# Kernel tuning notes

Measured on AMD Instinct MI355X. Metric: run time of the kernel, lower is better.

The kernel has to match this reference:

```python
import jax, jax.numpy as jnp
import numpy as np

CAM_DIM = 3          # args().cam_dim
ROT_DIM = 6          # args().rot_dim
NJ = 22              # number of SMPL joints in the 6D pose slice
CENTER2D_THRESH = 5.0
POSE_THRESH = 2.5
N = 2048
BATCH = 32
MAP_SIZE = 64        # args().centermap_size
PARAM_DIM = CAM_DIM + NJ * ROT_DIM + 10  # 145


def rot6d_to_rotmat(x):
    """6D rotation rep -> rotation matrix via Gram-Schmidt (ROMP convention).
    x: [N, NJ*6] -> R: [N, NJ, 3, 3] (b1,b2,b3 as columns)."""
    x = x.reshape(-1, NJ, 3, 2)
    a1, a2 = x[..., 0], x[..., 1]
    b1 = a1 / jnp.linalg.norm(a1, axis=-1, keepdims=True)
    a2p = a2 - jnp.sum(b1 * a2, axis=-1, keepdims=True) * b1
    b2 = a2p / jnp.linalg.norm(a2p, axis=-1, keepdims=True)
    b3 = jnp.cross(b1, b2)
    return jnp.stack([b1, b2, b3], axis=-1)


def setup_inputs() -> dict:
    key = jax.random.key(0)
    k1, k2, k3, k4 = jax.random.split(key, 4)
    params_preds = jax.random.normal(k1, (N, PARAM_DIM), dtype=jnp.float32)
    pred_batch_ids = jax.random.randint(k2, (N,), 0, BATCH, dtype=jnp.int32)
    pred_czyxs = jax.random.randint(k3, (N, 3), 0, MAP_SIZE, dtype=jnp.int32)
    top_score = jax.random.uniform(k4, (N,), dtype=jnp.float32)
    return {"params_preds": params_preds, "pred_batch_ids": pred_batch_ids,
            "pred_czyxs": pred_czyxs, "top_score": top_score}


def reference(params_preds, pred_batch_ids, pred_czyxs, top_score):
    n = top_score.shape[0]
    pose6d = params_preds[:, CAM_DIM:CAM_DIM + NJ * ROT_DIM]

    # pairwise L2 distance of 2D centers (czyx[:,1:])
    centers = pred_czyxs[:, 1:].astype(jnp.float32)                 # [N,2]
    c_dist = jnp.linalg.norm(centers[:, None, :] - centers[None, :, :], axis=-1)
    same_batch = pred_batch_ids[:, None] == pred_batch_ids[None, :]
    c_dist = jnp.where(same_batch, c_dist, CENTER2D_THRESH + 1.0)
    similarity = c_dist <= CENTER2D_THRESH                          # [N,N] bool

    # pairwise SMPL pose L2 error: mean_j ||R_i[j] - R_k[j]||_F
    # (original goes 6D -> angle-axis -> rotmat; the roundtrip is the identity,
    #  so we compare the Gram-Schmidt rotation matrices directly)
    R = rot6d_to_rotmat(pose6d)                                     # [N,NJ,3,3]
    G = jnp.einsum('ikab,jkab->ijk', R, R)                          # [N,N,NJ]
    n2 = jnp.sum(R * R, axis=(-1, -2))                              # [N,NJ]
    d2 = jnp.clip(n2[:, None, :] + n2[None, :, :] - 2.0 * G, 0.0, None)
    pose_dist = jnp.sqrt(d2).mean(-1)                               # [N,N]

    # per-row pose suppression (vectorized form of the python loop; rows are
    # independent and the diagonal always survives since pose_dist[i,i]=0)
    similarity = similarity & (pose_dist < POSE_THRESH)

    score_map = similarity.astype(top_score.dtype) * top_score[None, :]
    nms_inds = jnp.argmax(score_map, axis=1) == jnp.arange(n)
    return score_map, nms_inds
```

## Files before the change

kernel.cpp:

```cpp
#include <hip/hip_runtime.h>

#define NJ 22
#define CAM_DIM 3

__device__ __forceinline__ void rot6(const float* __restrict__ p, float r[9]) {
    float a1x = p[0], a2x = p[1];
    float a1y = p[2], a2y = p[3];
    float a1z = p[4], a2z = p[5];
    float n1 = sqrtf(a1x*a1x + a1y*a1y + a1z*a1z);
    float b1x = a1x/n1, b1y = a1y/n1, b1z = a1z/n1;
    float d = b1x*a2x + b1y*a2y + b1z*a2z;
    float px = a2x - d*b1x, py = a2y - d*b1y, pz = a2z - d*b1z;
    float np = sqrtf(px*px + py*py + pz*pz);
    float b2x = px/np, b2y = py/np, b2z = pz/np;
    r[0]=b1x; r[1]=b1y; r[2]=b1z;
    r[3]=b2x; r[4]=b2y; r[5]=b2z;
    r[6]=b1y*b2z - b1z*b2y;
    r[7]=b1z*b2x - b1x*b2z;
    r[8]=b1x*b2y - b1y*b2x;
}

__global__ __launch_bounds__(256) void mega_kernel(
        const float* __restrict__ params,
        const int* __restrict__ batch_ids,
        const int* __restrict__ czyx,
        const float* __restrict__ ts,
        float* __restrict__ out,
        float* __restrict__ nms,
        int n, int param_dim) {
    __shared__ unsigned long long s_red[4];

    const int i    = blockIdx.x;
    const int tid  = threadIdx.x;
    const int lane = tid & 63;
    const int wid  = tid >> 6;

    const int bi  = batch_ids[i];
    const int ciy = czyx[3*i + 1];
    const int cix = czyx[3*i + 2];
    float* row = out + (size_t)i * n;

    unsigned long long best = 0ull;

    for (int base = 0; base < n; base += blockDim.x * 4) {
        int j0 = base + tid * 4;
        if (j0 >= n) continue;

        int okmask = 0;
        if (j0 + 3 < n) {
            int4 b4 = *reinterpret_cast<const int4*>(batch_ids + j0);
            const int4* cz = reinterpret_cast<const int4*>(czyx + 3*j0);
            int4 c0 = cz[0], c1 = cz[1], c2 = cz[2];
            int by[4] = {b4.x, b4.y, b4.z, b4.w};
            int yy[4] = {c0.y, c1.x, c1.w, c2.z};
            int xx[4] = {c0.z, c1.y, c2.x, c2.w};
            #pragma unroll
            for (int u = 0; u < 4; ++u) {
                int dy = yy[u] - ciy, dx = xx[u] - cix;
                if ((by[u] == bi) && (dy*dy + dx*dx <= 25)) okmask |= 1 << u;
            }
        } else {
            for (int u = 0; u < 4 && j0 + u < n; ++u) {
                int j = j0 + u;
                int dy = czyx[3*j + 1] - ciy, dx = czyx[3*j + 2] - cix;
                if ((batch_ids[j] == bi) && (dy*dy + dx*dx <= 25)) okmask |= 1 << u;
            }
        }

        int passmask = 0;
        int du = i - j0;
        if (du >= 0 && du < 4) {
            passmask |=  (1 << du);
            okmask   &= ~(1 << du);
        }

        for (;;) {
            unsigned long long pend = __ballot(okmask != 0);
            if (pend == 0ull) break;
            int leader = __ffsll((long long)pend) - 1;
            int lok = __shfl(okmask, leader);
            int u   = __ffs(lok) - 1;
            int j   = __shfl(j0, leader) + u;

            float val = 0.0f;
            if (lane < NJ) {
                const float* pi_ = params + (size_t)i * param_dim + CAM_DIM + lane * 6;
                const float* pj_ = params + (size_t)j * param_dim + CAM_DIM + lane * 6;
                float ri[9], rj[9];
                rot6(pi_, ri);
                rot6(pj_, rj);
                float g = 0.0f, ni = 0.0f, nj = 0.0f;
                #pragma unroll
                for (int a = 0; a < 9; ++a) {
                    g  += ri[a]*rj[a];
                    ni += ri[a]*ri[a];
                    nj += rj[a]*rj[a];
                }
                val = sqrtf(fmaxf(ni + nj - 2.0f*g, 0.0f));
            }
            #pragma unroll
            for (int off = 16; off > 0; off >>= 1) val += __shfl_down(val, off, 32);
            float pd = __shfl(val, 0) * (1.0f / 22.0f);

            if (lane == leader) {
                okmask &= ~(1 << u);
                if (pd < 2.5f) passmask |= 1 << u;
            }
        }

        float sc[4];
        #pragma unroll
        for (int u = 0; u < 4; ++u)
            sc[u] = ((passmask >> u) & 1) ? ts[j0 + u] : 0.0f;

        unsigned long long cand = (unsigned int)(~(unsigned int)j0);
        if (cand > best) best = cand;
        #pragma unroll
        for (int u = 0; u < 4; ++u) {
            if ((passmask >> u) & 1) {
                unsigned long long p =
                    ((unsigned long long)__float_as_uint(sc[u]) << 32) |
                    (unsigned int)(~(unsigned int)(j0 + u));
                if (p > best) best = p;
            }
        }

        if (j0 + 3 < n) {
            *reinterpret_cast<float4*>(row + j0) = make_float4(sc[0], sc[1], sc[2], sc[3]);
        } else {
            for (int u = 0; u < 4 && j0 + u < n; ++u) row[j0 + u] = sc[u];
        }
    }

    #pragma unroll
    for (int off = 32; off > 0; off >>= 1) {
        unsigned long long o = __shfl_xor(best, off);
        if (o > best) best = o;
    }
    if (lane == 0) s_red[wid] = best;
    __syncthreads();
    if (tid == 0) {
        unsigned long long b = s_red[0];
        #pragma unroll
        for (int w = 1; w < 4; ++w) if (s_red[w] > b) b = s_red[w];
        unsigned int jwin = ~(unsigned int)(b & 0xFFFFFFFFull);
        nms[i] = (jwin == (unsigned int)i) ? 1.0f : 0.0f;
    }
}

extern "C" void kernel_launch(void* const* d_in, const int* in_sizes, int n_in,
                              void* d_out, int out_size, void* d_ws, size_t ws_size,
                              hipStream_t stream) {
    const float* params = (const float*)d_in[0];
    const int*   batch  = (const int*)d_in[1];
    const int*   czyx   = (const int*)d_in[2];
    const float* ts     = (const float*)d_in[3];

    const int n = in_sizes[1];
    const int param_dim = in_sizes[0] / n;

    float* out = (float*)d_out;
    float* nms = out + (size_t)n * n;

    mega_kernel<<<n, 256, 0, stream>>>(params, batch, czyx, ts, out, nms, n, param_dim);
}
```

Baseline: 15.86 us.

## Split into gate and pose kernels with precomputed rotation matrices and hit lists

Splits the fused kernel into two. The first kernel builds each row's rotation matrices and squared norms once into workspace, writes gated scores, and records up to 64 spatial hits per row in a list. The second kernel, one wavefront per row, computes the pose distance only for those hits, zeroes suppressed entries and picks the NMS winner. This removes the repeated 6D-to-rotmat work and the wave-serialized pose loop from the bandwidth-bound output pass. In exchange it adds a second launch and workspace traffic, and rows with more than 64 hits would give wrong results.

```diff
diff --git a/kernel.cpp b/kernel.cpp
--- a/kernel.cpp
+++ b/kernel.cpp
@@ -2,6 +2,8 @@
 
 #define NJ 22
 #define CAM_DIM 3
+#define RSTRIDE 224
+#define HITCAP 64
 
 __device__ __forceinline__ void rot6(const float* __restrict__ p, float r[9]) {
     float a1x = p[0], a2x = p[1];
@@ -20,27 +22,39 @@
     r[8]=b1x*b2y - b1y*b2x;
 }
 
-__global__ __launch_bounds__(256) void mega_kernel(
+__global__ __launch_bounds__(256) void gate_kernel(
         const float* __restrict__ params,
         const int* __restrict__ batch_ids,
         const int* __restrict__ czyx,
         const float* __restrict__ ts,
         float* __restrict__ out,
-        float* __restrict__ nms,
+        float* __restrict__ ws_R,
+        int* __restrict__ ws_cnt,
+        int* __restrict__ ws_hits,
         int n, int param_dim) {
-    __shared__ unsigned long long s_red[4];
+    __shared__ int l_cnt;
+    __shared__ int l_hits[HITCAP];
 
-    const int i    = blockIdx.x;
-    const int tid  = threadIdx.x;
-    const int lane = tid & 63;
-    const int wid  = tid >> 6;
+    const int i   = blockIdx.x;
+    const int tid = threadIdx.x;
+
+    if (tid == 0) l_cnt = 0;
+
+    if (tid < NJ) {
+        float r[9];
+        rot6(params + (size_t)i * param_dim + CAM_DIM + tid * 6, r);
+        float* Ri = ws_R + (size_t)i * RSTRIDE;
+        float s = 0.0f;
+        #pragma unroll
+        for (int a = 0; a < 9; ++a) { Ri[tid*9 + a] = r[a]; s += r[a]*r[a]; }
+        Ri[198 + tid] = s;
+    }
+    __syncthreads();
 
     const int bi  = batch_ids[i];
     const int ciy = czyx[3*i + 1];
     const int cix = czyx[3*i + 2];
     float* row = out + (size_t)i * n;
-
-    unsigned long long best = 0ull;
 
     for (int base = 0; base < n; base += blockDim.x * 4) {
         int j0 = base + tid * 4;
@@ -67,83 +81,91 @@
             }
         }
 
-        int passmask = 0;
+        int pending = okmask;
         int du = i - j0;
-        if (du >= 0 && du < 4) {
-            passmask |=  (1 << du);
-            okmask   &= ~(1 << du);
-        }
-
-        for (;;) {
-            unsigned long long pend = __ballot(okmask != 0);
-            if (pend == 0ull) break;
-            int leader = __ffsll((long long)pend) - 1;
-            int lok = __shfl(okmask, leader);
-            int u   = __ffs(lok) - 1;
-            int j   = __shfl(j0, leader) + u;
-
-            float val = 0.0f;
-            if (lane < NJ) {
-                const float* pi_ = params + (size_t)i * param_dim + CAM_DIM + lane * 6;
-                const float* pj_ = params + (size_t)j * param_dim + CAM_DIM + lane * 6;
-                float ri[9], rj[9];
-                rot6(pi_, ri);
-                rot6(pj_, rj);
-                float g = 0.0f, ni = 0.0f, nj = 0.0f;
-                #pragma unroll
-                for (int a = 0; a < 9; ++a) {
-                    g  += ri[a]*rj[a];
-                    ni += ri[a]*ri[a];
-                    nj += rj[a]*rj[a];
-                }
-                val = sqrtf(fmaxf(ni + nj - 2.0f*g, 0.0f));
-            }
-            #pragma unroll
-            for (int off = 16; off > 0; off >>= 1) val += __shfl_down(val, off, 32);
-            float pd = __shfl(val, 0) * (1.0f / 22.0f);
-
-            if (lane == leader) {
-                okmask &= ~(1 << u);
-                if (pd < 2.5f) passmask |= 1 << u;
-            }
-        }
+        if (du >= 0 && du < 4) pending &= ~(1 << du);
 
         float sc[4];
         #pragma unroll
         for (int u = 0; u < 4; ++u)
-            sc[u] = ((passmask >> u) & 1) ? ts[j0 + u] : 0.0f;
-
-        unsigned long long cand = (unsigned int)(~(unsigned int)j0);
-        if (cand > best) best = cand;
-        #pragma unroll
-        for (int u = 0; u < 4; ++u) {
-            if ((passmask >> u) & 1) {
-                unsigned long long p =
-                    ((unsigned long long)__float_as_uint(sc[u]) << 32) |
-                    (unsigned int)(~(unsigned int)(j0 + u));
-                if (p > best) best = p;
-            }
-        }
+            sc[u] = ((okmask >> u) & 1) ? ts[j0 + u] : 0.0f;
 
         if (j0 + 3 < n) {
             *reinterpret_cast<float4*>(row + j0) = make_float4(sc[0], sc[1], sc[2], sc[3]);
         } else {
             for (int u = 0; u < 4 && j0 + u < n; ++u) row[j0 + u] = sc[u];
         }
+
+        while (pending) {
+            int u = __ffs(pending) - 1;
+            pending &= pending - 1;
+            int pos = atomicAdd(&l_cnt, 1);
+            if (pos < HITCAP) l_hits[pos] = j0 + u;
+        }
     }
 
-    #pragma unroll
-    for (int off = 32; off > 0; off >>= 1) {
-        unsigned long long o = __shfl_xor(best, off);
-        if (o > best) best = o;
+    __syncthreads();
+    int cnt = l_cnt < HITCAP ? l_cnt : HITCAP;
+    if (tid == 0) ws_cnt[i] = cnt;
+    for (int t = tid; t < cnt; t += blockDim.x) ws_hits[i * HITCAP + t] = l_hits[t];
+}
+
+__global__ __launch_bounds__(64) void pose_kernel(
+        const float* __restrict__ ts,
+        const float* __restrict__ ws_R,
+        const int* __restrict__ ws_cnt,
+        const int* __restrict__ ws_hits,
+        float* __restrict__ out,
+        float* __restrict__ nms,
+        int n) {
+    const int i    = blockIdx.x;
+    const int lane = threadIdx.x;
+
+    const int cnt = ws_cnt[i];
+
+    float ri[9];
+    float n2i = 0.0f;
+    if (lane < NJ) {
+        const float* Ri = ws_R + (size_t)i * RSTRIDE;
+        #pragma unroll
+        for (int a = 0; a < 9; ++a) ri[a] = Ri[lane*9 + a];
+        n2i = Ri[198 + lane];
     }
-    if (lane == 0) s_red[wid] = best;
-    __syncthreads();
-    if (tid == 0) {
-        unsigned long long b = s_red[0];
+
+    unsigned long long best =
+        ((unsigned long long)__float_as_uint(ts[i]) << 32) | (unsigned int)(~(unsigned int)i);
+    unsigned long long zfloor = (unsigned int)0xFFFFFFFFu;
+    if (zfloor > best) best = zfloor;
+
+    for (int h = 0; h < cnt; ++h) {
+        int j = ws_hits[i * HITCAP + h];
+        float val = 0.0f;
+        if (lane < NJ) {
+            const float* Rj = ws_R + (size_t)j * RSTRIDE;
+            float g = 0.0f;
+            #pragma unroll
+            for (int a = 0; a < 9; ++a) g += ri[a] * Rj[lane*9 + a];
+            float d2 = fmaxf(n2i + Rj[198 + lane] - 2.0f * g, 0.0f);
+            val = sqrtf(d2);
+        }
         #pragma unroll
-        for (int w = 1; w < 4; ++w) if (s_red[w] > b) b = s_red[w];
-        unsigned int jwin = ~(unsigned int)(b & 0xFFFFFFFFull);
+        for (int off = 16; off > 0; off >>= 1) val += __shfl_down(val, off, 32);
+        float pd = __shfl(val, 0) * (1.0f / 22.0f);
+
+        if (lane == 0) {
+            if (pd < 2.5f) {
+                unsigned long long p =
+                    ((unsigned long long)__float_as_uint(ts[j]) << 32) |
+                    (unsigned int)(~(unsigned int)j);
+                if (p > best) best = p;
+            } else {
+                out[(size_t)i * n + j] = 0.0f;
+            }
+        }
+    }
+
+    if (lane == 0) {
+        unsigned int jwin = ~(unsigned int)(best & 0xFFFFFFFFull);
         nms[i] = (jwin == (unsigned int)i) ? 1.0f : 0.0f;
     }
 }
@@ -159,8 +181,14 @@
     const int n = in_sizes[1];
     const int param_dim = in_sizes[0] / n;
 
+    float* ws_R    = (float*)d_ws;
+    int*   ws_cnt  = (int*)(ws_R + (size_t)n * RSTRIDE);
+    int*   ws_hits = ws_cnt + n;
+
     float* out = (float*)d_out;
     float* nms = out + (size_t)n * n;
 
-    mega_kernel<<<n, 256, 0, stream>>>(params, batch, czyx, ts, out, nms, n, param_dim);
+    gate_kernel<<<n, 256, 0, stream>>>(params, batch, czyx, ts, out,
+                                       ws_R, ws_cnt, ws_hits, n, param_dim);
+    pose_kernel<<<n, 64, 0, stream>>>(ts, ws_R, ws_cnt, ws_hits, out, nms, n);
 }
```

Measured after the change: 18.23 us. 14.9% more time.

## Map one wavefront per row and hoist row-i rotation out of pair loop

Applied to the files above, without the earlier changes.

Each wavefront now owns one output row and walks all columns in chunks of 256, instead of a whole 256-thread block sharing one row. This removes the shared-memory and __syncthreads reduction for the argmax. The row's rotation matrices and their squared norms are computed once per lane before the loop, so candidate pairs only evaluate rot6 for the column. The trade-off is less parallelism per row: one wave serialises the candidate processing that four waves previously split.

```diff
diff --git a/kernel.cpp b/kernel.cpp
--- a/kernel.cpp
+++ b/kernel.cpp
@@ -20,7 +20,7 @@
     r[8]=b1x*b2y - b1y*b2x;
 }
 
-__global__ __launch_bounds__(256) void mega_kernel(
+__global__ __launch_bounds__(256) void row_kernel(
         const float* __restrict__ params,
         const int* __restrict__ batch_ids,
         const int* __restrict__ czyx,
@@ -28,23 +28,28 @@
         float* __restrict__ out,
         float* __restrict__ nms,
         int n, int param_dim) {
-    __shared__ unsigned long long s_red[4];
+    const int lane = threadIdx.x & 63;
+    const int wid  = threadIdx.x >> 6;
+    const int r    = blockIdx.x * 4 + wid;
+    if (r >= n) return;
 
-    const int i    = blockIdx.x;
-    const int tid  = threadIdx.x;
-    const int lane = tid & 63;
-    const int wid  = tid >> 6;
+    const int bi  = batch_ids[r];
+    const int ciy = czyx[3*r + 1];
+    const int cix = czyx[3*r + 2];
+    float* row = out + (size_t)r * n;
 
-    const int bi  = batch_ids[i];
-    const int ciy = czyx[3*i + 1];
-    const int cix = czyx[3*i + 2];
-    float* row = out + (size_t)i * n;
+    float ri[9];
+    float n2i = 0.0f;
+    if (lane < NJ) {
+        rot6(params + (size_t)r * param_dim + CAM_DIM + lane * 6, ri);
+        #pragma unroll
+        for (int a = 0; a < 9; ++a) n2i += ri[a] * ri[a];
+    }
 
     unsigned long long best = 0ull;
 
-    for (int base = 0; base < n; base += blockDim.x * 4) {
-        int j0 = base + tid * 4;
-        if (j0 >= n) continue;
+    for (int c = 0; c < n; c += 256) {
+        int j0 = c + lane * 4;
 
         int okmask = 0;
         if (j0 + 3 < n) {
@@ -68,7 +73,7 @@
         }
 
         int passmask = 0;
-        int du = i - j0;
+        int du = r - j0;
         if (du >= 0 && du < 4) {
             passmask |=  (1 << du);
             okmask   &= ~(1 << du);
@@ -84,19 +89,15 @@
 
             float val = 0.0f;
             if (lane < NJ) {
-                const float* pi_ = params + (size_t)i * param_dim + CAM_DIM + lane * 6;
-                const float* pj_ = params + (size_t)j * param_dim + CAM_DIM + lane * 6;
-                float ri[9], rj[9];
-                rot6(pi_, ri);
-                rot6(pj_, rj);
-                float g = 0.0f, ni = 0.0f, nj = 0.0f;
+                float rj[9];
+                rot6(params + (size_t)j * param_dim + CAM_DIM + lane * 6, rj);
+                float g = 0.0f, nj = 0.0f;
                 #pragma unroll
                 for (int a = 0; a < 9; ++a) {
-                    g  += ri[a]*rj[a];
-                    ni += ri[a]*ri[a];
-                    nj += rj[a]*rj[a];
+                    g  += ri[a] * rj[a];
+                    nj += rj[a] * rj[a];
                 }
-                val = sqrtf(fmaxf(ni + nj - 2.0f*g, 0.0f));
+                val = sqrtf(fmaxf(n2i + nj - 2.0f*g, 0.0f));
             }
             #pragma unroll
             for (int off = 16; off > 0; off >>= 1) val += __shfl_down(val, off, 32);
@@ -137,14 +138,9 @@
         unsigned long long o = __shfl_xor(best, off);
         if (o > best) best = o;
     }
-    if (lane == 0) s_red[wid] = best;
-    __syncthreads();
-    if (tid == 0) {
-        unsigned long long b = s_red[0];
-        #pragma unroll
-        for (int w = 1; w < 4; ++w) if (s_red[w] > b) b = s_red[w];
-        unsigned int jwin = ~(unsigned int)(b & 0xFFFFFFFFull);
-        nms[i] = (jwin == (unsigned int)i) ? 1.0f : 0.0f;
+    if (lane == 0) {
+        unsigned int jwin = ~(unsigned int)(best & 0xFFFFFFFFull);
+        nms[r] = (jwin == (unsigned int)r) ? 1.0f : 0.0f;
     }
 }
 
@@ -162,5 +158,7 @@
     float* out = (float*)d_out;
     float* nms = out + (size_t)n * n;
 
-    mega_kernel<<<n, 256, 0, stream>>>(params, batch, czyx, ts, out, nms, n, param_dim);
+    int blocks = (n + 3) / 4;
+    row_kernel<<<blocks, 256, 0, stream>>>(params, batch, czyx, ts,
+                                           out, nms, n, param_dim);
 }
```

After: 19.54 us. 23.2% more time.

## Split each score row across a 2D grid and reduce argmax in a second kernel

Applied to the files above, without the earlier changes.

The single per-row block that looped over all columns becomes a 2D grid, where each block handles one 1024-column chunk of one row. That doubles the number of independent blocks and removes the in-block column loop. Each wave writes its packed (score, index) maximum to workspace, and a small second kernel reduces those partials into the NMS flags. Score loads for the store are now vectorized as float4 alongside the gating loads. The cost is an extra kernel launch and a round trip through global memory for the partials.

```diff
diff --git a/kernel.cpp b/kernel.cpp
--- a/kernel.cpp
+++ b/kernel.cpp
@@ -20,115 +20,113 @@
     r[8]=b1x*b2y - b1y*b2x;
 }
 
-__global__ __launch_bounds__(256) void mega_kernel(
+__global__ __launch_bounds__(256) void gate_store_kernel(
         const float* __restrict__ params,
         const int* __restrict__ batch_ids,
         const int* __restrict__ czyx,
         const float* __restrict__ ts,
         float* __restrict__ out,
-        float* __restrict__ nms,
+        unsigned long long* __restrict__ partials,
         int n, int param_dim) {
-    __shared__ unsigned long long s_red[4];
-
-    const int i    = blockIdx.x;
+    const int i    = blockIdx.y;
     const int tid  = threadIdx.x;
     const int lane = tid & 63;
     const int wid  = tid >> 6;
+    const int j0   = blockIdx.x * (blockDim.x * 4) + tid * 4;
 
     const int bi  = batch_ids[i];
     const int ciy = czyx[3*i + 1];
     const int cix = czyx[3*i + 2];
-    float* row = out + (size_t)i * n;
 
-    unsigned long long best = 0ull;
-
-    for (int base = 0; base < n; base += blockDim.x * 4) {
-        int j0 = base + tid * 4;
-        if (j0 >= n) continue;
-
-        int okmask = 0;
-        if (j0 + 3 < n) {
-            int4 b4 = *reinterpret_cast<const int4*>(batch_ids + j0);
-            const int4* cz = reinterpret_cast<const int4*>(czyx + 3*j0);
-            int4 c0 = cz[0], c1 = cz[1], c2 = cz[2];
-            int by[4] = {b4.x, b4.y, b4.z, b4.w};
-            int yy[4] = {c0.y, c1.x, c1.w, c2.z};
-            int xx[4] = {c0.z, c1.y, c2.x, c2.w};
-            #pragma unroll
-            for (int u = 0; u < 4; ++u) {
-                int dy = yy[u] - ciy, dx = xx[u] - cix;
-                if ((by[u] == bi) && (dy*dy + dx*dx <= 25)) okmask |= 1 << u;
-            }
-        } else {
-            for (int u = 0; u < 4 && j0 + u < n; ++u) {
-                int j = j0 + u;
-                int dy = czyx[3*j + 1] - ciy, dx = czyx[3*j + 2] - cix;
-                if ((batch_ids[j] == bi) && (dy*dy + dx*dx <= 25)) okmask |= 1 << u;
-            }
-        }
-
-        int passmask = 0;
-        int du = i - j0;
-        if (du >= 0 && du < 4) {
-            passmask |=  (1 << du);
-            okmask   &= ~(1 << du);
-        }
-
-        for (;;) {
-            unsigned long long pend = __ballot(okmask != 0);
-            if (pend == 0ull) break;
-            int leader = __ffsll((long long)pend) - 1;
-            int lok = __shfl(okmask, leader);
-            int u   = __ffs(lok) - 1;
-            int j   = __shfl(j0, leader) + u;
-
-            float val = 0.0f;
-            if (lane < NJ) {
-                const float* pi_ = params + (size_t)i * param_dim + CAM_DIM + lane * 6;
-                const float* pj_ = params + (size_t)j * param_dim + CAM_DIM + lane * 6;
-                float ri[9], rj[9];
-                rot6(pi_, ri);
-                rot6(pj_, rj);
-                float g = 0.0f, ni = 0.0f, nj = 0.0f;
-                #pragma unroll
-                for (int a = 0; a < 9; ++a) {
-                    g  += ri[a]*rj[a];
-                    ni += ri[a]*ri[a];
-                    nj += rj[a]*rj[a];
-                }
-                val = sqrtf(fmaxf(ni + nj - 2.0f*g, 0.0f));
-            }
-            #pragma unroll
-            for (int off = 16; off > 0; off >>= 1) val += __shfl_down(val, off, 32);
-            float pd = __shfl(val, 0) * (1.0f / 22.0f);
-
-            if (lane == leader) {
-                okmask &= ~(1 << u);
-                if (pd < 2.5f) passmask |= 1 << u;
-            }
-        }
-
-        float sc[4];
-        #pragma unroll
-        for (int u = 0; u < 4; ++u)
-            sc[u] = ((passmask >> u) & 1) ? ts[j0 + u] : 0.0f;
-
-        unsigned long long cand = (unsigned int)(~(unsigned int)j0);
-        if (cand > best) best = cand;
+    int okmask = 0;
+    float tsv[4] = {0.f, 0.f, 0.f, 0.f};
+    if (j0 + 3 < n) {
+        int4 b4 = *reinterpret_cast<const int4*>(batch_ids + j0);
+        const int4* cz = reinterpret_cast<const int4*>(czyx + 3*j0);
+        int4 c0 = cz[0], c1 = cz[1], c2 = cz[2];
+        float4 t = *reinterpret_cast<const float4*>(ts + j0);
+        int by[4] = {b4.x, b4.y, b4.z, b4.w};
+        int yy[4] = {c0.y, c1.x, c1.w, c2.z};
+        int xx[4] = {c0.z, c1.y, c2.x, c2.w};
+        tsv[0]=t.x; tsv[1]=t.y; tsv[2]=t.z; tsv[3]=t.w;
         #pragma unroll
         for (int u = 0; u < 4; ++u) {
-            if ((passmask >> u) & 1) {
-                unsigned long long p =
-                    ((unsigned long long)__float_as_uint(sc[u]) << 32) |
-                    (unsigned int)(~(unsigned int)(j0 + u));
-                if (p > best) best = p;
+            int dy = yy[u] - ciy, dx = xx[u] - cix;
+            if ((by[u] == bi) && (dy*dy + dx*dx <= 25)) okmask |= 1 << u;
+        }
+    } else {
+        for (int u = 0; u < 4 && j0 + u < n; ++u) {
+            int j = j0 + u;
+            int dy = czyx[3*j + 1] - ciy, dx = czyx[3*j + 2] - cix;
+            tsv[u] = ts[j];
+            if ((batch_ids[j] == bi) && (dy*dy + dx*dx <= 25)) okmask |= 1 << u;
+        }
+    }
+
+    int passmask = 0;
+    int du = i - j0;
+    if (du >= 0 && du < 4) {
+        passmask |=  (1 << du) & okmask;
+        okmask   &= ~(1 << du);
+    } else {
+        okmask = okmask;
+    }
+    int pending = okmask & ~passmask;
+
+    for (;;) {
+        unsigned long long pend = __ballot(pending != 0);
+        if (pend == 0ull) break;
+        int leader = __ffsll((long long)pend) - 1;
+        int lok = __shfl(pending, leader);
+        int u   = __ffs(lok) - 1;
+        int j   = __shfl(j0, leader) + u;
+
+        float val = 0.0f;
+        if (lane < NJ) {
+            const float* pi_ = params + (size_t)i * param_dim + CAM_DIM + lane * 6;
+            const float* pj_ = params + (size_t)j * param_dim + CAM_DIM + lane * 6;
+            float ri[9], rj[9];
+            rot6(pi_, ri);
+            rot6(pj_, rj);
+            float g = 0.0f, ni = 0.0f, nj = 0.0f;
+            #pragma unroll
+            for (int a = 0; a < 9; ++a) {
+                g  += ri[a]*rj[a];
+                ni += ri[a]*ri[a];
+                nj += rj[a]*rj[a];
             }
+            val = sqrtf(fmaxf(ni + nj - 2.0f*g, 0.0f));
         }
+        #pragma unroll
+        for (int off = 16; off > 0; off >>= 1) val += __shfl_down(val, off, 32);
+        float pd = __shfl(val, 0) * (1.0f / 22.0f);
 
-        if (j0 + 3 < n) {
-            *reinterpret_cast<float4*>(row + j0) = make_float4(sc[0], sc[1], sc[2], sc[3]);
-        } else {
-            for (int u = 0; u < 4 && j0 + u < n; ++u) row[j0 + u] = sc[u];
+        if (lane == leader) {
+            pending &= ~(1 << u);
+            if (pd < 2.5f) passmask |= 1 << u;
+        }
+    }
+
+    float sc[4];
+    #pragma unroll
+    for (int u = 0; u < 4; ++u)
+        sc[u] = ((passmask >> u) & 1) ? tsv[u] : 0.0f;
+
+    if (j0 + 3 < n) {
+        *reinterpret_cast<float4*>(out + (size_t)i * n + j0) =
+            make_float4(sc[0], sc[1], sc[2], sc[3]);
+    } else {
+        for (int u = 0; u < 4 && j0 + u < n; ++u) out[(size_t)i * n + j0 + u] = sc[u];
+    }
+
+    unsigned long long best = (unsigned int)(~(unsigned int)j0);
+    #pragma unroll
+    for (int u = 0; u < 4; ++u) {
+        if ((passmask >> u) & 1) {
+            unsigned long long p =
+                ((unsigned long long)__float_as_uint(sc[u]) << 32) |
+                (unsigned int)(~(unsigned int)(j0 + u));
+            if (p > best) best = p;
         }
     }
 
@@ -137,15 +135,24 @@
         unsigned long long o = __shfl_xor(best, off);
         if (o > best) best = o;
     }
-    if (lane == 0) s_red[wid] = best;
-    __syncthreads();
-    if (tid == 0) {
-        unsigned long long b = s_red[0];
-        #pragma unroll
-        for (int w = 1; w < 4; ++w) if (s_red[w] > b) b = s_red[w];
-        unsigned int jwin = ~(unsigned int)(b & 0xFFFFFFFFull);
-        nms[i] = (jwin == (unsigned int)i) ? 1.0f : 0.0f;
+    if (lane == 0) {
+        int nwpb   = blockDim.x >> 6;
+        int nppr   = gridDim.x * nwpb;
+        partials[(size_t)i * nppr + blockIdx.x * nwpb + wid] = best;
     }
+}
+
+__global__ void nms_kernel(const unsigned long long* __restrict__ partials,
+                           float* __restrict__ nms, int n, int nppr) {
+    int i = blockIdx.x * blockDim.x + threadIdx.x;
+    if (i >= n) return;
+    unsigned long long b = partials[(size_t)i * nppr];
+    for (int p = 1; p < nppr; ++p) {
+        unsigned long long o = partials[(size_t)i * nppr + p];
+        if (o > b) b = o;
+    }
+    unsigned int jwin = ~(unsigned int)(b & 0xFFFFFFFFull);
+    nms[i] = (jwin == (unsigned int)i) ? 1.0f : 0.0f;
 }
 
 extern "C" void kernel_launch(void* const* d_in, const int* in_sizes, int n_in,
@@ -161,6 +168,12 @@
 
     float* out = (float*)d_out;
     float* nms = out + (size_t)n * n;
+    unsigned long long* partials = (unsigned long long*)d_ws;
 
-    mega_kernel<<<n, 256, 0, stream>>>(params, batch, czyx, ts, out, nms, n, param_dim);
+    int gx   = (n + 1023) / 1024;
+    int nppr = gx * 4;
+    dim3 grid(gx, n);
+    gate_store_kernel<<<grid, 256, 0, stream>>>(params, batch, czyx, ts,
+                                                out, partials, n, param_dim);
+    nms_kernel<<<(n + 255) / 256, 256, 0, stream>>>(partials, nms, n, nppr);
 }
```

New measurement: 17.49 us. 1.1x slower.
